# Kernel tuning notes

Hardware: AMD Instinct MI355X
Metric: run time of the kernel (lower is better)

Reference implementation:

```python
import jax, jax.numpy as jnp
import numpy as np

H = 56; W = 56; WS = 7; SS = 3; HEADS = 12; DIM = 384
N = WS * WS; NW = (H // WS) * (W // WS); EPS = 1e-5


def _attn_mask():
    img = np.zeros((H, W), np.float32)
    cnt = 0
    for hs in (slice(0, -WS), slice(-WS, -SS), slice(-SS, None)):
        for ws in (slice(0, -WS), slice(-WS, -SS), slice(-SS, None)):
            img[hs, ws] = cnt
            cnt += 1
    m = img.reshape(H // WS, WS, W // WS, WS).transpose(0, 2, 1, 3).reshape(-1, N)
    d = m[:, None, :] - m[:, :, None]
    return jnp.asarray(np.where(d != 0, -100.0, 0.0).astype(np.float32))


def _rel_coords():
    c = np.stack(np.meshgrid(np.arange(WS), np.arange(WS), indexing='ij')).reshape(2, -1)
    rel = (c[:, :, None] - c[:, None, :]).astype(np.float32)
    rel = np.sign(rel) * np.log1p(np.abs(rel))
    return jnp.asarray(np.stack([rel[0], rel[1]], -1).reshape(-1, 2))


ATTN_MASK = _attn_mask()  # (NW, N, N)
REL = _rel_coords()       # (N*N, 2)


def _ln(x, g, b):
    mu = x.mean(-1, keepdims=True)
    var = ((x - mu) ** 2).mean(-1, keepdims=True)
    return (x - mu) / jnp.sqrt(var + EPS) * g + b


def setup_inputs() -> dict:
    key = jax.random.key(0)
    ks = jax.random.split(key, 8)
    s = 0.02
    B = 32
    return {
        'x': jax.random.normal(ks[0], (B, H * W, DIM), jnp.float32),
        'norm1_g': jnp.ones((DIM,), jnp.float32),
        'norm1_b': jnp.zeros((DIM,), jnp.float32),
        'qkv_w': jax.random.normal(ks[1], (DIM, 3 * DIM), jnp.float32) * s,
        'qkv_b': jnp.zeros((3 * DIM,), jnp.float32),
        'tau': jnp.ones((HEADS,), jnp.float32),
        'proj_w': jax.random.normal(ks[2], (DIM, DIM), jnp.float32) * s,
        'proj_b': jnp.zeros((DIM,), jnp.float32),
        'crpb_w1': jax.random.normal(ks[3], (2, 64), jnp.float32) * s,
        'crpb_b1': jnp.zeros((64,), jnp.float32),
        'crpb_w2': jax.random.normal(ks[4], (64, HEADS), jnp.float32) * s,
        'crpb_b2': jnp.zeros((HEADS,), jnp.float32),
        'norm2_g': jnp.ones((DIM,), jnp.float32),
        'norm2_b': jnp.zeros((DIM,), jnp.float32),
        'mlp_w1': jax.random.normal(ks[5], (DIM, 4 * DIM), jnp.float32) * s,
        'mlp_b1': jnp.zeros((4 * DIM,), jnp.float32),
        'mlp_w2': jax.random.normal(ks[6], (4 * DIM, DIM), jnp.float32) * s,
        'mlp_b2': jnp.zeros((DIM,), jnp.float32),
    }


def reference(x, norm1_g, norm1_b, qkv_w, qkv_b, tau, proj_w, proj_b,
              crpb_w1, crpb_b1, crpb_w2, crpb_b2, norm2_g, norm2_b,
              mlp_w1, mlp_b1, mlp_w2, mlp_b2):
    B = x.shape[0]
    shortcut = x
    h = _ln(x, norm1_g, norm1_b).reshape(B, H, W, DIM)
    # cyclic shift
    h = jnp.roll(h, (-SS, -SS), axis=(1, 2))
    # window partition -> (B*NW, N, DIM)
    xw = h.reshape(B, H // WS, WS, W // WS, WS, DIM).transpose(0, 1, 3, 2, 4, 5).reshape(-1, N, DIM)
    qkv = xw @ qkv_w + qkv_b
    q, k, v = jnp.split(qkv, 3, axis=-1)
    hd = DIM // HEADS
    def to_heads(t):
        return t.reshape(-1, N, HEADS, hd).transpose(0, 2, 1, 3)  # (Bw, heads, N, hd)
    q, k, v = to_heads(q), to_heads(k), to_heads(v)
    q = q / jnp.maximum(jnp.linalg.norm(q, axis=-1, keepdims=True), 1e-12)
    k = k / jnp.maximum(jnp.linalg.norm(k, axis=-1, keepdims=True), 1e-12)
    attn = jnp.einsum('whnd,whmd->whnm', q, k) * tau[None, :, None, None]
    # continuous relative position bias
    bias = jax.nn.relu(REL @ crpb_w1 + crpb_b1) @ crpb_w2 + crpb_b2  # (N*N, heads)
    bias = bias.reshape(N, N, HEADS).transpose(2, 0, 1)
    attn = attn + bias[None]
    attn = attn.reshape(B, NW, HEADS, N, N) + ATTN_MASK[None, :, None]
    attn = jax.nn.softmax(attn.reshape(-1, HEADS, N, N), axis=-1)
    out = jnp.einsum('whnm,whmd->whnd', attn, v).transpose(0, 2, 1, 3).reshape(-1, N, DIM)
    out = out @ proj_w + proj_b
    # window reverse
    h = out.reshape(B, H // WS, W // WS, WS, WS, DIM).transpose(0, 1, 3, 2, 4, 5).reshape(B, H, W, DIM)
    h = jnp.roll(h, (SS, SS), axis=(1, 2)).reshape(B, H * W, DIM)
    x = shortcut + h
    m = _ln(x, norm2_g, norm2_b)
    m = jax.nn.gelu(m @ mlp_w1 + mlp_b1, approximate=False) @ mlp_w2 + mlp_b2
    return x + m
```

## Files before the change

### kernel.cpp

```cpp
#include <hip/hip_runtime.h>
#include <cstdint>
#include <cstddef>


typedef unsigned short u16;
typedef __bf16 bf16x8 __attribute__((ext_vector_type(8)));
typedef float f32x4 __attribute__((ext_vector_type(4)));

#define VMW8 asm volatile("s_waitcnt vmcnt(8)" ::: "memory")
#define VMW0 asm volatile("s_waitcnt vmcnt(0)" ::: "memory")
#define LGKM0 asm volatile("s_waitcnt lgkmcnt(0)" ::: "memory")

__device__ __forceinline__ u16 f2bf(float f) {
  unsigned u = __builtin_bit_cast(unsigned, f);
  u += 0x7fffu + ((u >> 16) & 1u);
  return (u16)(u >> 16);
}

__device__ __forceinline__ void gll16(const u16* g, u16* l) {
  __builtin_amdgcn_global_load_lds(
      (const __attribute__((address_space(1))) void*)g,
      (__attribute__((address_space(3))) void*)l, 16, 0, 0);
}

__global__ __launch_bounds__(256) void fill_k(float* o, int n) {
  int i = blockIdx.x * 256 + threadIdx.x;
  if (i < n) o[i] = 12345.0f;
}

__global__ __launch_bounds__(256) void wconv_k(
    const float* __restrict__ qkv_w, const float* __restrict__ proj_w,
    const float* __restrict__ mlp_w1, const float* __restrict__ mlp_w2,
    u16* __restrict__ o) {
  const int id = blockIdx.x * 256 + threadIdx.x;
  if (id < 442368) {
    const int n = id / 384, k = id - n * 384;
    o[id] = f2bf(qkv_w[k * 1152 + n]);
  } else if (id < 589824) {
    const int e = id - 442368; const int n = e / 384, k = e - n * 384;
    o[id] = f2bf(proj_w[k * 384 + n]);
  } else if (id < 1179648) {
    const int e = id - 589824; const int n = e / 384, k = e - n * 384;
    o[id] = f2bf(mlp_w1[k * 1536 + n]);
  } else {
    const int e = id - 1179648; const int n = e / 1536, k = e - n * 1536;
    o[id] = f2bf(mlp_w2[k * 384 + n]);
  }
}

__global__ __launch_bounds__(256) void biastab_k(
    const float* __restrict__ w1, const float* __restrict__ b1,
    const float* __restrict__ w2, const float* __restrict__ b2,
    float* __restrict__ biasT) {
  const int id = blockIdx.x * 256 + threadIdx.x;
  if (id >= 2401) return;
  const int i = id / 49, j = id - i * 49;
  const int r1 = i / 7, c1 = i - r1 * 7, r2 = j / 7, c2 = j - r2 * 7;
  float dy = (float)(r1 - r2), dx = (float)(c1 - c2);
  dy = copysignf(log1pf(fabsf(dy)), dy);
  dx = copysignf(log1pf(fabsf(dx)), dx);
  float accv[12];
#pragma unroll
  for (int t = 0; t < 12; ++t) accv[t] = b2[t];
  for (int u = 0; u < 64; ++u) {
    float hu = fmaxf(dy * w1[u] + dx * w1[64 + u] + b1[u], 0.0f);
#pragma unroll
    for (int t = 0; t < 12; ++t) accv[t] += hu * w2[u * 12 + t];
  }
#pragma unroll
  for (int t = 0; t < 12; ++t) biasT[t * 2401 + id] = accv[t];
}

template <int WINMAP>
__global__ __launch_bounds__(256, 4) void ln_k(
    const float* __restrict__ X, const float* __restrict__ g,
    const float* __restrict__ b, u16* __restrict__ O) {
  const int t = blockIdx.x * 4 + (threadIdx.x >> 6);
  const int lane = threadIdx.x & 63;
  const float* xr = X + (size_t)t * 384;
  float v[6];
  float s = 0.f;
#pragma unroll
  for (int i = 0; i < 6; ++i) { v[i] = xr[lane + i * 64]; s += v[i]; }
#pragma unroll
  for (int m = 1; m < 64; m <<= 1) s += __shfl_xor(s, m);
  const float mu = s * (1.0f / 384.0f);
  float q = 0.f;
#pragma unroll
  for (int i = 0; i < 6; ++i) { float d = v[i] - mu; q += d * d; }
#pragma unroll
  for (int m = 1; m < 64; m <<= 1) q += __shfl_xor(q, m);
  const float rstd = rsqrtf(q * (1.0f / 384.0f) + 1e-5f);
  size_t row;
  if constexpr (WINMAP) {
    const int bb = t / 3136, hw = t - bb * 3136;
    const int ho = hw / 56, wo = hw - ho * 56;
    int hs = ho - 3; if (hs < 0) hs += 56;
    int ws2 = wo - 3; if (ws2 < 0) ws2 += 56;
    const int h7 = hs / 7, w7 = ws2 / 7;
    const int wwin = bb * 64 + h7 * 8 + w7;
    const int p = (hs - h7 * 7) * 7 + (ws2 - w7 * 7);
    row = (size_t)wwin * 49 + p;
  } else {
    row = (size_t)t;
  }
  u16* orow = O + row * 384;
#pragma unroll
  for (int i = 0; i < 6; ++i) {
    const int d = lane + i * 64;
    orow[d] = f2bf((v[i] - mu) * rstd * g[d] + b[d]);
  }
}

template <int EPI>
__global__ __launch_bounds__(64, 2) void gemm_k(
    const u16* __restrict__ A, const u16* __restrict__ Bt,
    const float* __restrict__ bias, const float* __restrict__ aux,
    void* __restrict__ outp, int M, int N, int K) {
  __shared__ u16 Abuf[2][2048];
  __shared__ u16 Bbuf[2][2048];
  const int lane = threadIdx.x;
  const int l15 = lane & 15, l4 = lane >> 4;

  const int nx = gridDim.x;
  const int nwg = nx * gridDim.y;
  int bid = blockIdx.y * nx + blockIdx.x;
  bid = (bid & 7) * (nwg >> 3) + (bid >> 3);
  const int tileN = (bid % nx) * 64;
  const int tileM = (bid / nx) * 64;

  const int prow_l = lane >> 2;
  const int lrow_l = prow_l ^ ((prow_l >> 2) & 1);
  const int lslot = (lane & 3) ^ (lrow_l & 3);
  const u16* Ag = A + (size_t)(tileM + lrow_l) * K + lslot * 8;
  const u16* Bg = Bt + (size_t)(tileN + lrow_l) * K + lslot * 8;
  const size_t cstrideA = (size_t)16 * K;

  f32x4 acc[4][4] = {};

#define STAGE(k0, b)                                             \
  {                                                              \
    _Pragma("unroll") for (int c = 0; c < 4; ++c) {              \
      gll16(Ag + (size_t)c * cstrideA + (k0), &Abuf[b][c * 512]);\
      gll16(Bg + (size_t)c * cstrideA + (k0), &Bbuf[b][c * 512]);\
    }                                                            \
  }

#define COMPUTE(b)                                                        \
  {                                                                       \
    bf16x8 af[4], bfr[4];                                                 \
    _Pragma("unroll") for (int f = 0; f < 4; ++f) {                       \
      const int R = f * 16 + l15;                                         \
      const int off = (R * 32 + 8 * l4) ^ ((R & 7) << 3);                 \
      af[f] = *(const bf16x8*)&Abuf[b][off];                              \
      bfr[f] = *(const bf16x8*)&Bbuf[b][off];                             \
    }                                                                     \
    __builtin_amdgcn_s_setprio(1);                                        \
    _Pragma("unroll") for (int fm = 0; fm < 4; ++fm)                      \
        _Pragma("unroll") for (int fn = 0; fn < 4; ++fn) acc[fm][fn] =    \
            __builtin_amdgcn_mfma_f32_16x16x32_bf16(af[fm], bfr[fn],      \
                                                    acc[fm][fn], 0, 0, 0);\
    __builtin_amdgcn_s_setprio(0);                                        \
  }

  const int nt = K >> 5;
  STAGE(0, 0);
  STAGE(32, 1);
  for (int t = 0; t + 2 < nt; ++t) {
    VMW8;
    COMPUTE(t & 1);
    LGKM0;
    STAGE((size_t)(t + 2) * 32, t & 1);
  }
  VMW8;
  COMPUTE(nt & 1);
  VMW0;
  COMPUTE((nt - 1) & 1);
#undef STAGE
#undef COMPUTE

  if constexpr (EPI == 0) {
    u16* O = (u16*)outp;
#pragma unroll
    for (int fm = 0; fm < 4; ++fm) {
#pragma unroll
      for (int hp = 0; hp < 2; ++hp) {
        const int c0e = tileN + hp * 32;
        const int seg = c0e >> 5;
        const bool nrm = seg < 24;
        const float tfac = (seg < 12) ? aux[seg] : 1.0f;
        const float b0 = bias[c0e + l15];
        const float b1 = bias[c0e + 16 + l15];
#pragma unroll
        for (int r = 0; r < 4; ++r) {
          float v0 = acc[fm][2 * hp][r] + b0;
          float v1 = acc[fm][2 * hp + 1][r] + b1;
          if (nrm) {
            float ss = v0 * v0 + v1 * v1;
            ss += __shfl_xor(ss, 1);
            ss += __shfl_xor(ss, 2);
            ss += __shfl_xor(ss, 4);
            ss += __shfl_xor(ss, 8);
            const float f = tfac / fmaxf(sqrtf(ss), 1e-12f);
            v0 *= f; v1 *= f;
          }
          const size_t row = (size_t)(tileM + fm * 16 + l4 * 4 + r);
          O[row * N + c0e + l15] = f2bf(v0);
          O[row * N + c0e + 16 + l15] = f2bf(v1);
        }
      }
    }
  } else if constexpr (EPI == 1) {
    float* O = (float*)outp;
    const float* X = aux;
#pragma unroll
    for (int fm = 0; fm < 4; ++fm) {
#pragma unroll
      for (int r = 0; r < 4; ++r) {
        const int row = tileM + fm * 16 + l4 * 4 + r;
        const int w = row / 49, p = row - w * 49;
        const int bb = w >> 6, widx = w & 63;
        const int p7 = p / 7;
        int hs = (widx >> 3) * 7 + p7;
        int ws2 = (widx & 7) * 7 + (p - p7 * 7);
        int ho = hs + 3; if (ho >= 56) ho -= 56;
        int wo = ws2 + 3; if (wo >= 56) wo -= 56;
        const size_t tok = (size_t)bb * 3136 + ho * 56 + wo;
#pragma unroll
        for (int fn = 0; fn < 4; ++fn) {
          const int col = tileN + fn * 16 + l15;
          O[tok * 384 + col] = X[tok * 384 + col] + acc[fm][fn][r] + bias[col];
        }
      }
    }
  } else if constexpr (EPI == 2) {
    u16* O = (u16*)outp;
#pragma unroll
    for (int fm = 0; fm < 4; ++fm) {
#pragma unroll
      for (int fn = 0; fn < 4; ++fn) {
        const int col = tileN + fn * 16 + l15;
        const float bc = bias[col];
#pragma unroll
        for (int r = 0; r < 4; ++r) {
          const size_t row = (size_t)(tileM + fm * 16 + l4 * 4 + r);
          const float v = acc[fm][fn][r] + bc;
          const float g = 0.5f * v * (1.0f + erff(v * 0.70710678118654752f));
          O[row * N + col] = f2bf(g);
        }
      }
    }
  } else {
    float* O = (float*)outp;
#pragma unroll
    for (int fm = 0; fm < 4; ++fm) {
#pragma unroll
      for (int fn = 0; fn < 4; ++fn) {
        const int col = tileN + fn * 16 + l15;
        const float bc = bias[col];
#pragma unroll
        for (int r = 0; r < 4; ++r) {
          const size_t row = (size_t)(tileM + fm * 16 + l4 * 4 + r);
          O[row * N + col] += acc[fm][fn][r] + bc;
        }
      }
    }
  }
}

__global__ __launch_bounds__(256, 2) void attn_k(
    const u16* __restrict__ qkv, const float* __restrict__ biasT,
    u16* __restrict__ outp) {
  __shared__ u16 lds[4][7552];
  const int tid = threadIdx.x, lane = tid & 63, wid = tid >> 6;
  const int l15 = lane & 15, l4 = lane >> 4;
  const int W = blockIdx.x * 4 + wid;
  const int w = W / 12, h = W - w * 12;
  u16* S = lds[wid];
  u16* Q = S;
  u16* Kl = S + 2560;
  u16* P = S;
  u16* VT = S + 5120;
  float* sums = (float*)(S + 7424);
  const u16* base = qkv + (size_t)w * 56448 + h * 32;
  const int widx = w & 63, wh = widx >> 3, ww = widx & 7;
  const bool masked = (wh == 7) || (ww == 7);

#pragma unroll
  for (int it = 0; it < 4; ++it) {
    const int row = it * 16 + (lane >> 2);
    const int c8 = (lane & 3) * 8;
    uint4 qv = {0, 0, 0, 0}, kv = {0, 0, 0, 0};
    if (row < 49) {
      qv = *(const uint4*)(base + (size_t)row * 1152 + c8);
      kv = *(const uint4*)(base + (size_t)row * 1152 + 384 + c8);
    }
    *(uint4*)&Q[row * 40 + c8] = qv;
    *(uint4*)&Kl[row * 40 + c8] = kv;
  }
  {
    const int d = lane & 31;
    const int jh = lane >> 5;
#pragma unroll 4
    for (int jt = 0; jt < 32; ++jt) {
      const int j = jt * 2 + jh;
      u16 val = 0;
      if (j < 49) val = base[(size_t)j * 1152 + 768 + d];
      VT[d * 72 + j] = val;
    }
  }
  LGKM0;

  f32x4 sc[4][4] = {};
  {
    bf16x8 aq[4], bk[4];
#pragma unroll
    for (int f = 0; f < 4; ++f)
      aq[f] = *(const bf16x8*)&Q[(f * 16 + l15) * 40 + 8 * l4];
#pragma unroll
    for (int f = 0; f < 4; ++f)
      bk[f] = *(const bf16x8*)&Kl[(f * 16 + l15) * 40 + 8 * l4];
    __builtin_amdgcn_s_setprio(1);
#pragma unroll
    for (int fm = 0; fm < 4; ++fm)
#pragma unroll
      for (int fn = 0; fn < 4; ++fn)
        sc[fm][fn] = __builtin_amdgcn_mfma_f32_16x16x32_bf16(
            aq[fm], bk[fn], sc[fm][fn], 0, 0, 0);
    __builtin_amdgcn_s_setprio(0);
  }
  LGKM0;

  int codej[4] = {0, 0, 0, 0};
  if (masked) {
#pragma unroll
    for (int fn = 0; fn < 4; ++fn) {
      const int j = fn * 16 + l15;
      const int pr = j / 7, pc = j - pr * 7;
      const int rr2 = (wh == 7) ? ((pr < 4) ? 1 : 2) : 0;
      const int cc2 = (ww == 7) ? ((pc < 4) ? 1 : 2) : 0;
      codej[fn] = rr2 * 3 + cc2;
    }
  }
#pragma unroll
  for (int fm = 0; fm < 4; ++fm) {
#pragma unroll
    for (int r = 0; r < 4; ++r) {
      const int i = fm * 16 + l4 * 4 + r;
      const bool iok = i < 49;
      int ci = 0;
      if (masked && iok) {
        const int pr = i / 7, pc = i - pr * 7;
        const int rr2 = (wh == 7) ? ((pr < 4) ? 1 : 2) : 0;
        const int cc2 = (ww == 7) ? ((pc < 4) ? 1 : 2) : 0;
        ci = rr2 * 3 + cc2;
      }
      const float* brow = biasT + (size_t)h * 2401 + (iok ? i : 0) * 49;
      float sv[4];
#pragma unroll
      for (int fn = 0; fn < 4; ++fn) {
        const int j = fn * 16 + l15;
        float s = sc[fm][fn][r];
        if (iok && j < 49) {
          s += brow[j];
          if (masked && codej[fn] != ci) s -= 100.0f;
        } else {
          s = -1e30f;
        }
        sv[fn] = s;
      }
      float mx = fmaxf(fmaxf(sv[0], sv[1]), fmaxf(sv[2], sv[3]));
      mx = fmaxf(mx, __shfl_xor(mx, 1));
      mx = fmaxf(mx, __shfl_xor(mx, 2));
      mx = fmaxf(mx, __shfl_xor(mx, 4));
      mx = fmaxf(mx, __shfl_xor(mx, 8));
      float sm = 0.f;
      u16 pb[4];
#pragma unroll
      for (int fn = 0; fn < 4; ++fn) {
        const float e = __expf(sv[fn] - mx);
        sm += e;
        pb[fn] = f2bf(e);
      }
      sm += __shfl_xor(sm, 1);
      sm += __shfl_xor(sm, 2);
      sm += __shfl_xor(sm, 4);
      sm += __shfl_xor(sm, 8);
#pragma unroll
      for (int fn = 0; fn < 4; ++fn) P[i * 72 + fn * 16 + l15] = pb[fn];
      if (l15 == 0) sums[i] = sm;
    }
  }
  LGKM0;

  f32x4 o[4][2] = {};
#pragma unroll
  for (int kk = 0; kk < 2; ++kk) {
    bf16x8 pa[4], bv[2];
#pragma unroll
    for (int fm = 0; fm < 4; ++fm)
      pa[fm] = *(const bf16x8*)&P[(fm * 16 + l15) * 72 + kk * 32 + 8 * l4];
#pragma unroll
    for (int fn = 0; fn < 2; ++fn)
      bv[fn] = *(const bf16x8*)&VT[(fn * 16 + l15) * 72 + kk * 32 + 8 * l4];
    __builtin_amdgcn_s_setprio(1);
#pragma unroll
    for (int fm = 0; fm < 4; ++fm)
#pragma unroll
      for (int fn = 0; fn < 2; ++fn)
        o[fm][fn] = __builtin_amdgcn_mfma_f32_16x16x32_bf16(
            pa[fm], bv[fn], o[fm][fn], 0, 0, 0);
    __builtin_amdgcn_s_setprio(0);
  }
  u16* ob = outp + (size_t)w * 49 * 384 + h * 32;
#pragma unroll
  for (int fm = 0; fm < 4; ++fm) {
#pragma unroll
    for (int r = 0; r < 4; ++r) {
      const int i = fm * 16 + l4 * 4 + r;
      if (i < 49) {
        const float inv = 1.0f / sums[i];
        ob[(size_t)i * 384 + l15] = f2bf(o[fm][0][r] * inv);
        ob[(size_t)i * 384 + 16 + l15] = f2bf(o[fm][1][r] * inv);
      }
    }
  }
}

extern "C" void kernel_launch(void* const* d_in, const int* in_sizes, int n_in,
                              void* d_out, int out_size, void* d_ws,
                              size_t ws_size, hipStream_t stream) {
  const float* x      = (const float*)d_in[0];
  const float* n1g    = (const float*)d_in[1];
  const float* n1b    = (const float*)d_in[2];
  const float* qkv_w  = (const float*)d_in[3];
  const float* qkv_b  = (const float*)d_in[4];
  const float* tau    = (const float*)d_in[5];
  const float* proj_w = (const float*)d_in[6];
  const float* proj_b = (const float*)d_in[7];
  const float* c_w1   = (const float*)d_in[8];
  const float* c_b1   = (const float*)d_in[9];
  const float* c_w2   = (const float*)d_in[10];
  const float* c_b2   = (const float*)d_in[11];
  const float* n2g    = (const float*)d_in[12];
  const float* n2b    = (const float*)d_in[13];
  const float* mlp_w1 = (const float*)d_in[14];
  const float* mlp_b1 = (const float*)d_in[15];
  const float* mlp_w2 = (const float*)d_in[16];
  const float* mlp_b2 = (const float*)d_in[17];
  float* out = (float*)d_out;
  char* ws = (char*)d_ws;

  constexpr size_t WS_WT    = 0;
  constexpr size_t WS_BIAST = 3538944;
  constexpr size_t WS_XW    = 4194304;
  constexpr size_t WS_QKV   = 81264640;
  constexpr size_t WS_ATT   = 312475648;
  constexpr size_t WS_NEED  = 389545984;

  if (ws_size < WS_NEED) {
    fill_k<<<(out_size + 255) / 256, 256, 0, stream>>>(out, out_size);
    return;
  }

  u16* wqkvT  = (u16*)(ws + WS_WT);
  u16* wprojT = (u16*)(ws + WS_WT + 884736);
  u16* wm1T   = (u16*)(ws + WS_WT + 1179648);
  u16* wm2T   = (u16*)(ws + WS_WT + 2359296);
  float* biasT = (float*)(ws + WS_BIAST);
  u16* xw  = (u16*)(ws + WS_XW);
  u16* qkv = (u16*)(ws + WS_QKV);
  u16* att = (u16*)(ws + WS_ATT);
  u16* hid = qkv;
  u16* ln2 = xw;

  wconv_k<<<6912, 256, 0, stream>>>(qkv_w, proj_w, mlp_w1, mlp_w2, (u16*)ws);
  biastab_k<<<10, 256, 0, stream>>>(c_w1, c_b1, c_w2, c_b2, biasT);
  ln_k<1><<<25088, 256, 0, stream>>>(x, n1g, n1b, xw);
  gemm_k<0><<<dim3(18, 1568), 64, 0, stream>>>(xw, wqkvT, qkv_b, tau, qkv,
                                               100352, 1152, 384);
  attn_k<<<6144, 256, 0, stream>>>(qkv, biasT, att);
  gemm_k<1><<<dim3(6, 1568), 64, 0, stream>>>(att, wprojT, proj_b, x, out,
                                              100352, 384, 384);
  ln_k<0><<<25088, 256, 0, stream>>>(out, n2g, n2b, ln2);
  gemm_k<2><<<dim3(24, 1568), 64, 0, stream>>>(ln2, wm1T, mlp_b1, nullptr, hid,
                                               100352, 1536, 384);
  gemm_k<3><<<dim3(6, 1568), 64, 0, stream>>>(hid, wm2T, mlp_b2, nullptr, out,
                                              100352, 384, 1536);
}
```

Before: 1.729 ms.

## Use 128x128 four-wave GEMM tiles with triple-buffered LDS pipeline

Restructures the GEMM kernel from one wave per 64x64 tile to four waves sharing a 128x128 tile. Each wave loads a slice of the shared A/B panels and computes a 64x64 quadrant. The loads run through a three-stage LDS ring with barriers, and K becomes a compile-time template parameter. This is meant to double operand reuse from LDS, cut global traffic per FLOP, and hide load latency further ahead. In exchange it adds workgroup barriers and more LDS per block, which may limit occupancy.

```diff
diff --git a/kernel.cpp b/kernel.cpp
--- a/kernel.cpp
+++ b/kernel.cpp
@@ -8,8 +8,10 @@
 typedef float f32x4 __attribute__((ext_vector_type(4)));
 
 #define VMW8 asm volatile("s_waitcnt vmcnt(8)" ::: "memory")
+#define VMW4 asm volatile("s_waitcnt vmcnt(4)" ::: "memory")
 #define VMW0 asm volatile("s_waitcnt vmcnt(0)" ::: "memory")
 #define LGKM0 asm volatile("s_waitcnt lgkmcnt(0)" ::: "memory")
+#define BAR asm volatile("s_barrier" ::: "memory")
 
 __device__ __forceinline__ u16 f2bf(float f) {
   unsigned u = __builtin_bit_cast(unsigned, f);
@@ -112,48 +114,52 @@
   }
 }
 
-template <int EPI>
-__global__ __launch_bounds__(64, 2) void gemm_k(
+template <int EPI, int KK>
+__global__ __launch_bounds__(256, 3) void gemm_k(
     const u16* __restrict__ A, const u16* __restrict__ Bt,
     const float* __restrict__ bias, const float* __restrict__ aux,
-    void* __restrict__ outp, int M, int N, int K) {
-  __shared__ u16 Abuf[2][2048];
-  __shared__ u16 Bbuf[2][2048];
-  const int lane = threadIdx.x;
+    void* __restrict__ outp, int M, int N) {
+  __shared__ u16 Ab[3][4096];
+  __shared__ u16 Bb[3][4096];
+  const int tid = threadIdx.x;
+  const int lane = tid & 63;
+  const int wv = tid >> 6;
+  const int wrow = wv >> 1, wcol = wv & 1;
   const int l15 = lane & 15, l4 = lane >> 4;
 
   const int nx = gridDim.x;
   const int nwg = nx * gridDim.y;
   int bid = blockIdx.y * nx + blockIdx.x;
   bid = (bid & 7) * (nwg >> 3) + (bid >> 3);
-  const int tileN = (bid % nx) * 64;
-  const int tileM = (bid / nx) * 64;
-
-  const int prow_l = lane >> 2;
-  const int lrow_l = prow_l ^ ((prow_l >> 2) & 1);
-  const int lslot = (lane & 3) ^ (lrow_l & 3);
-  const u16* Ag = A + (size_t)(tileM + lrow_l) * K + lslot * 8;
-  const u16* Bg = Bt + (size_t)(tileN + lrow_l) * K + lslot * 8;
-  const size_t cstrideA = (size_t)16 * K;
+  const int tileN = (bid % nx) * 128;
+  const int tileM = (bid / nx) * 128;
+
+  const int prow = lane >> 2;
+  const int lrow = prow ^ ((prow >> 2) & 1);
+  const int lslot = (lane & 3) ^ (lrow & 3);
+  const u16* Ag = A + (size_t)(tileM + wv * 16 + lrow) * KK + lslot * 8;
+  const u16* Bg = Bt + (size_t)(tileN + wv * 16 + lrow) * KK + lslot * 8;
+  const size_t skip = (size_t)64 * KK;
 
   f32x4 acc[4][4] = {};
 
-#define STAGE(k0, b)                                             \
-  {                                                              \
-    _Pragma("unroll") for (int c = 0; c < 4; ++c) {              \
-      gll16(Ag + (size_t)c * cstrideA + (k0), &Abuf[b][c * 512]);\
-      gll16(Bg + (size_t)c * cstrideA + (k0), &Bbuf[b][c * 512]);\
-    }                                                            \
+#define STAGE(t, b)                                       \
+  {                                                       \
+    const size_t ko = (size_t)(t) * 32;                   \
+    gll16(Ag + ko, &Ab[b][wv * 512]);                     \
+    gll16(Ag + skip + ko, &Ab[b][(4 + wv) * 512]);        \
+    gll16(Bg + ko, &Bb[b][wv * 512]);                     \
+    gll16(Bg + skip + ko, &Bb[b][(4 + wv) * 512]);        \
   }
 
 #define COMPUTE(b)                                                        \
   {                                                                       \
     bf16x8 af[4], bfr[4];                                                 \
     _Pragma("unroll") for (int f = 0; f < 4; ++f) {                       \
-      const int R = f * 16 + l15;                                         \
-      const int off = (R * 32 + 8 * l4) ^ ((R & 7) << 3);                 \
-      af[f] = *(const bf16x8*)&Abuf[b][off];                              \
-      bfr[f] = *(const bf16x8*)&Bbuf[b][off];                             \
+      const int Ra = wrow * 64 + f * 16 + l15;                            \
+      const int Rb = wcol * 64 + f * 16 + l15;                            \
+      af[f] = *(const bf16x8*)&Ab[b][(Ra * 32 + 8 * l4) ^ ((Ra & 7) << 3)];\
+      bfr[f] = *(const bf16x8*)&Bb[b][(Rb * 32 + 8 * l4) ^ ((Rb & 7) << 3)];\
     }                                                                     \
     __builtin_amdgcn_s_setprio(1);                                        \
     _Pragma("unroll") for (int fm = 0; fm < 4; ++fm)                      \
@@ -163,29 +169,40 @@
     __builtin_amdgcn_s_setprio(0);                                        \
   }
 
-  const int nt = K >> 5;
+  constexpr int nt = KK >> 5;
   STAGE(0, 0);
-  STAGE(32, 1);
-  for (int t = 0; t + 2 < nt; ++t) {
+  STAGE(1, 1);
+  int cur = 0, nxt = 2;
+#pragma unroll 3
+  for (int t = 0; t < nt - 2; ++t) {
+    STAGE(t + 2, nxt);
     VMW8;
-    COMPUTE(t & 1);
-    LGKM0;
-    STAGE((size_t)(t + 2) * 32, t & 1);
-  }
-  VMW8;
-  COMPUTE(nt & 1);
+    BAR;
+    COMPUTE(cur);
+    BAR;
+    cur = (cur == 2) ? 0 : cur + 1;
+    nxt = (nxt == 2) ? 0 : nxt + 1;
+  }
+  VMW4;
+  BAR;
+  COMPUTE(cur);
+  cur = (cur == 2) ? 0 : cur + 1;
   VMW0;
-  COMPUTE((nt - 1) & 1);
+  BAR;
+  COMPUTE(cur);
 #undef STAGE
 #undef COMPUTE
 
+  const int baseRow = tileM + wrow * 64;
+  const int baseCol = tileN + wcol * 64;
+
   if constexpr (EPI == 0) {
     u16* O = (u16*)outp;
 #pragma unroll
     for (int fm = 0; fm < 4; ++fm) {
 #pragma unroll
       for (int hp = 0; hp < 2; ++hp) {
-        const int c0e = tileN + hp * 32;
+        const int c0e = baseCol + hp * 32;
         const int seg = c0e >> 5;
         const bool nrm = seg < 24;
         const float tfac = (seg < 12) ? aux[seg] : 1.0f;
@@ -204,7 +221,7 @@
             const float f = tfac / fmaxf(sqrtf(ss), 1e-12f);
             v0 *= f; v1 *= f;
           }
-          const size_t row = (size_t)(tileM + fm * 16 + l4 * 4 + r);
+          const size_t row = (size_t)(baseRow + fm * 16 + l4 * 4 + r);
           O[row * N + c0e + l15] = f2bf(v0);
           O[row * N + c0e + 16 + l15] = f2bf(v1);
         }
@@ -217,7 +234,7 @@
     for (int fm = 0; fm < 4; ++fm) {
 #pragma unroll
       for (int r = 0; r < 4; ++r) {
-        const int row = tileM + fm * 16 + l4 * 4 + r;
+        const int row = baseRow + fm * 16 + l4 * 4 + r;
         const int w = row / 49, p = row - w * 49;
         const int bb = w >> 6, widx = w & 63;
         const int p7 = p / 7;
@@ -228,7 +245,7 @@
         const size_t tok = (size_t)bb * 3136 + ho * 56 + wo;
 #pragma unroll
         for (int fn = 0; fn < 4; ++fn) {
-          const int col = tileN + fn * 16 + l15;
+          const int col = baseCol + fn * 16 + l15;
           O[tok * 384 + col] = X[tok * 384 + col] + acc[fm][fn][r] + bias[col];
         }
       }
@@ -239,11 +256,11 @@
     for (int fm = 0; fm < 4; ++fm) {
 #pragma unroll
       for (int fn = 0; fn < 4; ++fn) {
-        const int col = tileN + fn * 16 + l15;
+        const int col = baseCol + fn * 16 + l15;
         const float bc = bias[col];
 #pragma unroll
         for (int r = 0; r < 4; ++r) {
-          const size_t row = (size_t)(tileM + fm * 16 + l4 * 4 + r);
+          const size_t row = (size_t)(baseRow + fm * 16 + l4 * 4 + r);
           const float v = acc[fm][fn][r] + bc;
           const float g = 0.5f * v * (1.0f + erff(v * 0.70710678118654752f));
           O[row * N + col] = f2bf(g);
@@ -256,11 +273,11 @@
     for (int fm = 0; fm < 4; ++fm) {
 #pragma unroll
       for (int fn = 0; fn < 4; ++fn) {
-        const int col = tileN + fn * 16 + l15;
+        const int col = baseCol + fn * 16 + l15;
         const float bc = bias[col];
 #pragma unroll
         for (int r = 0; r < 4; ++r) {
-          const size_t row = (size_t)(tileM + fm * 16 + l4 * 4 + r);
+          const size_t row = (size_t)(baseRow + fm * 16 + l4 * 4 + r);
           O[row * N + col] += acc[fm][fn][r] + bc;
         }
       }
@@ -477,14 +494,14 @@
   wconv_k<<<6912, 256, 0, stream>>>(qkv_w, proj_w, mlp_w1, mlp_w2, (u16*)ws);
   biastab_k<<<10, 256, 0, stream>>>(c_w1, c_b1, c_w2, c_b2, biasT);
   ln_k<1><<<25088, 256, 0, stream>>>(x, n1g, n1b, xw);
-  gemm_k<0><<<dim3(18, 1568), 64, 0, stream>>>(xw, wqkvT, qkv_b, tau, qkv,
-                                               100352, 1152, 384);
+  gemm_k<0, 384><<<dim3(9, 784), 256, 0, stream>>>(xw, wqkvT, qkv_b, tau, qkv,
+                                                   100352, 1152);
   attn_k<<<6144, 256, 0, stream>>>(qkv, biasT, att);
-  gemm_k<1><<<dim3(6, 1568), 64, 0, stream>>>(att, wprojT, proj_b, x, out,
-                                              100352, 384, 384);
+  gemm_k<1, 384><<<dim3(3, 784), 256, 0, stream>>>(att, wprojT, proj_b, x, out,
+                                                   100352, 384);
   ln_k<0><<<25088, 256, 0, stream>>>(out, n2g, n2b, ln2);
-  gemm_k<2><<<dim3(24, 1568), 64, 0, stream>>>(ln2, wm1T, mlp_b1, nullptr, hid,
-                                               100352, 1536, 384);
-  gemm_k<3><<<dim3(6, 1568), 64, 0, stream>>>(hid, wm2T, mlp_b2, nullptr, out,
-                                              100352, 384, 1536);
-}
+  gemm_k<2, 384><<<dim3(12, 784), 256, 0, stream>>>(ln2, wm1T, mlp_b1, nullptr,
+                                                    hid, 100352, 1536);
+  gemm_k<3, 1536><<<dim3(3, 784), 256, 0, stream>>>(hid, wm2T, mlp_b2, nullptr,
+                                                    out, 100352, 384);
+}
```

Measured after the change: 1.427 ms. -17.5%, faster.
